# Kernel optimization log

Hardware: AMD Instinct MI355X
Metric: run time of the kernel (lower is better)

## Reference

```python
import jax, jax.numpy as jnp
import numpy as np

B = 1024      # Monte-Carlo samples (batch)
NX, NY = 8, 8 # lattice size
I = 3         # local Hilbert dim (hole, down, up)
H = 256       # hidden_dim
N_TARGET = 48 # target particle number
SZ = 0        # target magnetization sector


def setup_inputs() -> dict:
    key = jax.random.key(0)
    ks = jax.random.split(key, 8)
    f = jnp.float32
    samples = jax.random.randint(ks[0], (B, NX, NY), 0, 3)
    s_in = 1.0 / np.sqrt(2 * H)
    W1 = jax.random.normal(ks[1], (2 * I, 2 * H, H), f) * s_in
    W2 = jax.random.normal(ks[2], (2 * I, 2 * H, H), f) * s_in
    Wmerge = jax.random.normal(ks[3], (2 * H, H), f) * s_in
    b1 = jnp.full((H,), 0.01, f)
    b2 = jnp.full((H,), 0.01, f)
    s_l = 1.0 / np.sqrt(H)
    Wl1 = jax.random.normal(ks[4], (H, I), f) * s_l
    bl1 = jnp.zeros((I,), f)
    Wl2 = jax.random.normal(ks[5], (H, I), f) * s_l
    bl2 = jnp.zeros((I,), f)
    return {"samples": samples, "W1": W1, "b1": b1, "W2": W2, "b2": b2,
            "Wmerge": Wmerge, "Wl1": Wl1, "bl1": bl1, "Wl2": Wl2, "bl2": bl2}


def _gru_cell(sx, sy, hx, hy, W1, b1, W2, b2, Wmerge):
    # sx,sy: [B,I] one-hot neighbor inputs; hx,hy: [B,H] neighbor hiddens
    st = jnp.concatenate([hx, hy], axis=1)   # [B, 2H]
    inp = jnp.concatenate([sx, sy], axis=1)  # [B, 2I]
    # torch: einsum('ijk,lj->ikl', W, st) then einsum('li,ikl->lk', inp, .)
    pre1 = jnp.einsum('li,ijk,lj->lk', inp, W1, st)
    h_tilde = jnp.tanh(pre1 + b1)
    pre2 = jnp.einsum('li,ijk,lj->lk', inp, W2, st)
    u = jax.nn.sigmoid(pre2 + b2)
    return u * h_tilde + (1.0 - u) * (st @ Wmerge)


def _forward(samples, W1, b1, W2, b2, Wmerge, Wl1, bl1, Wl2, bl2):
    f = W1.dtype
    oh = jax.nn.one_hot(samples, I, dtype=f)  # [B,NX,NY,I]
    z_h = jnp.zeros((B, H), f)
    z_s = jnp.zeros((B, I), f)
    hid = {}
    bl_up = (N_TARGET + 2 * SZ) // 2
    bl_dn = (N_TARGET - 2 * SZ) // 2
    bl_hole = NX * NY - N_TARGET
    n_up = jnp.zeros((B,), f)
    n_dn = jnp.zeros((B,), f)
    log_a = jnp.zeros((B,), f)
    log_p = jnp.zeros((B,), f)
    k = 0  # number of already-sampled sites (static per step)
    for ny in range(NY):
        # snake (zig-zag) ordering over the 2D lattice
        xs = range(NX) if ny % 2 == 0 else range(NX - 1, -1, -1)
        dx = -1 if ny % 2 == 0 else 1
        for nx in xs:
            nxn = nx + dx
            sx = oh[:, nxn, ny] if 0 <= nxn < NX else z_s
            hx = hid.get((nxn, ny), z_h)
            sy = oh[:, nx, ny - 1] if ny > 0 else z_s
            hy = hid.get((nx, ny - 1), z_h)
            h = _gru_cell(sx, sy, hx, hy, W1, b1, W2, b2, Wmerge)
            hid[(nx, ny)] = h
            probs = jax.nn.softmax(h @ Wl1 + bl1, axis=1)          # [B,I]
            phase = jnp.pi * jax.nn.soft_sign(h @ Wl2 + bl2)       # [B,I]
            # enforce particle-number / magnetization sectors (heaviside masks)
            m_up = (bl_up - n_up > 0).astype(f)
            m_dn = (bl_dn - n_dn > 0).astype(f)
            m_hole = (bl_hole - (k - n_up - n_dn) > 0).astype(f)
            mask = jnp.stack([m_hole, m_dn, m_up], axis=1)         # [B,I]
            amp = probs * mask
            amp = amp / jnp.maximum(amp.sum(axis=1, keepdims=True), 1e-30)
            s = samples[:, nx, ny]
            sel = jax.nn.one_hot(s, I, dtype=f)
            log_a = log_a + jnp.log(jnp.clip((amp * sel).sum(axis=1), 1e-12))
            log_p = log_p + (phase * sel).sum(axis=1)
            n_up = n_up + (s == 2).astype(f)
            n_dn = n_dn + (s == 1).astype(f)
            k += 1
    return 0.5 * log_a, log_p


def reference(samples, W1, b1, W2, b2, Wmerge, Wl1, bl1, Wl2, bl2):
    return _forward(samples, W1, b1, W2, b2, Wmerge, Wl1, bl1, Wl2, bl2)
```

## Files before the change

kernel.cpp:

```cpp
#include <hip/hip_runtime.h>
#include <hip/hip_bf16.h>
#include <math.h>

#define Bsz 1024
#define Hd  256
#define MAXTILE 40
#define PERM_PER_CELL (MAXTILE*32)
#define WTSTRIDE (768*512)
#define GHALF (Bsz*768)
#define NPART 4

typedef short bf16x8 __attribute__((ext_vector_type(8)));
typedef float f32x4  __attribute__((ext_vector_type(4)));

__global__ __launch_bounds__(256)
void build_wc(const float* __restrict__ W1, const float* __restrict__ W2,
              const float* __restrict__ Wm,
              __hip_bfloat16* __restrict__ Wht, __hip_bfloat16* __restrict__ Wlt)
{
    size_t idx = (size_t)blockIdx.x * 256 + threadIdx.x;
    int k = (int)(idx & 511);
    size_t rem = idx >> 9;
    int col = (int)(rem % 768);
    int c = (int)(rem / 768);
    int a = c >> 2, b = c & 3;
    float v;
    if (col < 256) {
        v = ((a < 3) ? W1[(size_t)a * 512 * 256 + k * 256 + col] : 0.f)
          + ((b < 3) ? W1[(size_t)(3 + b) * 512 * 256 + k * 256 + col] : 0.f);
    } else if (col < 512) {
        int cc = col - 256;
        v = ((a < 3) ? W2[(size_t)a * 512 * 256 + k * 256 + cc] : 0.f)
          + ((b < 3) ? W2[(size_t)(3 + b) * 512 * 256 + k * 256 + cc] : 0.f);
    } else {
        v = Wm[(size_t)k * 256 + (col - 512)];
    }
    __hip_bfloat16 vh = __float2bfloat16(v);
    __hip_bfloat16 vl = __float2bfloat16(v - __bfloat162float(vh));
    Wht[idx] = vh;
    Wlt[idx] = vl;
}

__global__ __launch_bounds__(256)
void bucketize(const int* __restrict__ samples, int* __restrict__ perm,
               int* __restrict__ tiletab)
{
    const int cell = blockIdx.x;
    const int t = threadIdx.x;
    const int ny = cell >> 3, ixs = cell & 7;
    const int nx  = (ny & 1) ? (7 - ixs) : ixs;
    const int dx  = (ny & 1) ? 1 : -1;
    const int nxn = nx + dx;
    const bool hasX = (nxn >= 0) && (nxn < 8);
    const bool hasY = (ny > 0);
    const int sx_off = nxn * 8 + ny;
    const int sy_off = nx * 8 + ny - 1;

    __shared__ int hist[16], cursor[16];
    int* pcell = perm + (size_t)cell * PERM_PER_CELL;
    for (int i = t; i < PERM_PER_CELL; i += 256) pcell[i] = -1;
    if (t < 16) hist[t] = 0;
    __syncthreads();

    int myc[4];
#pragma unroll
    for (int q = 0; q < 4; q++) {
        int l = t * 4 + q;
        int a = hasX ? samples[l * 64 + sx_off] : 3;
        int b = hasY ? samples[l * 64 + sy_off] : 3;
        myc[q] = a * 4 + b;
        atomicAdd(&hist[myc[q]], 1);
    }
    __syncthreads();

    if (t == 0) {
        int tile = 0, row = 0;
        for (int c = 0; c < 16; c++) {
            cursor[c] = row;
            int nt = (hist[c] + 31) >> 5;
            for (int k = 0; k < nt; k++) tiletab[cell * MAXTILE + tile + k] = c;
            tile += nt;
            row  += nt * 32;
        }
        for (; tile < MAXTILE; tile++) tiletab[cell * MAXTILE + tile] = -1;
    }
    __syncthreads();

#pragma unroll
    for (int q = 0; q < 4; q++) {
        int l = t * 4 + q;
        int pos = atomicAdd(&cursor[myc[q]], 1);
        pcell[pos] = l;
    }
}

__global__ __launch_bounds__(256)
void gemm_mfma(const __hip_bfloat16* __restrict__ hxh, const __hip_bfloat16* __restrict__ hxl,
               const __hip_bfloat16* __restrict__ hyh, const __hip_bfloat16* __restrict__ hyl,
               const __hip_bfloat16* __restrict__ Wht, const __hip_bfloat16* __restrict__ Wlt,
               const int* __restrict__ perm, const int* __restrict__ tiletab,
               float* __restrict__ Gp, int cell, int kbeg, int kend)
{
    const int combo = tiletab[cell * MAXTILE + blockIdx.y];
    if (combo < 0) return;
    const int chunk = blockIdx.z;
    const int kbase = chunk << 7;
    const int lo = (kbeg > kbase) ? kbeg : kbase;
    const int hi = (kend < kbase + 128) ? kend : (kbase + 128);
    const int k0 = blockIdx.x * 64;
    const int* pr = perm + (size_t)cell * PERM_PER_CELL + blockIdx.y * 32;
    float* Gout = Gp + (size_t)chunk * GHALF;

    const int t  = threadIdx.x;
    const int w  = t >> 6;
    const int l  = t & 63;
    const int lr = l & 15;
    const int lg = l >> 4;

    __shared__ __align__(16) short Bh[64 * 128];
    __shared__ __align__(16) short Bl[64 * 128];

    f32x4 acc0 = {0.f, 0.f, 0.f, 0.f};
    f32x4 acc1 = {0.f, 0.f, 0.f, 0.f};

    if (lo < hi) {
        const __hip_bfloat16* baseH = Wht + (size_t)combo * WTSTRIDE + kbase;
        const __hip_bfloat16* baseL = Wlt + (size_t)combo * WTSTRIDE + kbase;
        for (int i = t; i < 1024; i += 256) {
            int c  = i >> 4;
            int kq = i & 15;
            int q  = c * 16 + (kq ^ (c & 7));
            ((uint4*)Bh)[q] = *(const uint4*)(baseH + (size_t)(k0 + c) * 512 + kq * 8);
            ((uint4*)Bl)[q] = *(const uint4*)(baseL + (size_t)(k0 + c) * 512 + kq * 8);
        }
        __syncthreads();

        const __hip_bfloat16* Hh = (chunk < 2) ? hxh : hyh;
        const __hip_bfloat16* Hl = (chunk < 2) ? hxl : hyl;
        const int hbase = kbase - ((chunk < 2) ? 0 : 256);
        const int r0 = pr[lr];
        const int r1 = pr[16 + lr];
        const int cB = w * 16 + lr;

#pragma unroll
        for (int ks = 0; ks < 4; ks++) {
            const int koff = hbase + ks * 32 + lg * 8;
            bf16x8 a0h = (r0 >= 0) ? *(const bf16x8*)(Hh + (size_t)r0 * Hd + koff) : (bf16x8)0;
            bf16x8 a0l = (r0 >= 0) ? *(const bf16x8*)(Hl + (size_t)r0 * Hd + koff) : (bf16x8)0;
            bf16x8 a1h = (r1 >= 0) ? *(const bf16x8*)(Hh + (size_t)r1 * Hd + koff) : (bf16x8)0;
            bf16x8 a1l = (r1 >= 0) ? *(const bf16x8*)(Hl + (size_t)r1 * Hd + koff) : (bf16x8)0;

            const int kq = ks * 4 + lg;
            const int q  = cB * 16 + (kq ^ (cB & 7));
            bf16x8 bh = ((const bf16x8*)Bh)[q];
            bf16x8 bl = ((const bf16x8*)Bl)[q];

            acc0 = __builtin_amdgcn_mfma_f32_16x16x32_bf16(a0h, bh, acc0, 0, 0, 0);
            acc0 = __builtin_amdgcn_mfma_f32_16x16x32_bf16(a0h, bl, acc0, 0, 0, 0);
            acc0 = __builtin_amdgcn_mfma_f32_16x16x32_bf16(a0l, bh, acc0, 0, 0, 0);
            acc1 = __builtin_amdgcn_mfma_f32_16x16x32_bf16(a1h, bh, acc1, 0, 0, 0);
            acc1 = __builtin_amdgcn_mfma_f32_16x16x32_bf16(a1h, bl, acc1, 0, 0, 0);
            acc1 = __builtin_amdgcn_mfma_f32_16x16x32_bf16(a1l, bh, acc1, 0, 0, 0);
        }
    }

    const int colA = k0 + w * 16 + lr;
#pragma unroll
    for (int reg = 0; reg < 4; reg++) {
        const int rl = 4 * lg + reg;
        int ra = pr[rl];
        if (ra >= 0) Gout[(size_t)ra * 768 + colA] = acc0[reg];
        int rb = pr[16 + rl];
        if (rb >= 0) Gout[(size_t)rb * 768 + colA] = acc1[reg];
    }
}

__global__ __launch_bounds__(256)
void combine_logprob(const float* __restrict__ Gp, const int* __restrict__ samples,
                     const float* __restrict__ b1, const float* __restrict__ b2,
                     const float* __restrict__ Wl1, const float* __restrict__ bl1,
                     const float* __restrict__ Wl2, const float* __restrict__ bl2,
                     __hip_bfloat16* __restrict__ houth, __hip_bfloat16* __restrict__ houtl,
                     float* __restrict__ acc, float* __restrict__ out,
                     int s_off, int kcell)
{
    const int l = blockIdx.x;
    const int k = threadIdx.x;
    const float* g0 = Gp + (size_t)l * 768;

    float pre1 = b1[k], pre2 = b2[k], mg = 0.f;
#pragma unroll
    for (int z = 0; z < NPART; z++) {
        const float* g = g0 + (size_t)z * GHALF;
        pre1 += g[k];
        pre2 += g[256 + k];
        mg   += g[512 + k];
    }
    float ht = tanhf(pre1);
    float u  = 1.0f / (1.0f + expf(-pre2));
    float h  = u * ht + (1.0f - u) * mg;
    __hip_bfloat16 hh = __float2bfloat16(h);
    __hip_bfloat16 hl = __float2bfloat16(h - __bfloat162float(hh));
    houth[(size_t)l * Hd + k] = hh;
    houtl[(size_t)l * Hd + k] = hl;

    float v[6];
    v[0] = h * Wl1[k * 3 + 0];
    v[1] = h * Wl1[k * 3 + 1];
    v[2] = h * Wl1[k * 3 + 2];
    v[3] = h * Wl2[k * 3 + 0];
    v[4] = h * Wl2[k * 3 + 1];
    v[5] = h * Wl2[k * 3 + 2];
#pragma unroll
    for (int m = 1; m < 64; m <<= 1)
#pragma unroll
        for (int i = 0; i < 6; i++) v[i] += __shfl_xor(v[i], m);

    __shared__ float red[4][6];
    if ((k & 63) == 0) {
#pragma unroll
        for (int i = 0; i < 6; i++) red[k >> 6][i] = v[i];
    }
    __syncthreads();

    if (k == 0) {
        float p1[3], p2[3];
#pragma unroll
        for (int i = 0; i < 3; i++) {
            p1[i] = red[0][i]     + red[1][i]     + red[2][i]     + red[3][i];
            p2[i] = red[0][3 + i] + red[1][3 + i] + red[2][3 + i] + red[3][3 + i];
        }
        float la, lp, nu, nd;
        if (kcell == 0) { la = 0.f; lp = 0.f; nu = 0.f; nd = 0.f; }
        else {
            la = acc[l];           lp = acc[Bsz + l];
            nu = acc[2 * Bsz + l]; nd = acc[3 * Bsz + l];
        }
        float z0 = p1[0] + bl1[0], z1 = p1[1] + bl1[1], z2 = p1[2] + bl1[2];
        float zm = fmaxf(z0, fmaxf(z1, z2));
        float e0 = expf(z0 - zm), e1 = expf(z1 - zm), e2 = expf(z2 - zm);
        float es = e0 + e1 + e2;
        float mh = (16.0f - ((float)kcell - nu - nd) > 0.0f) ? 1.0f : 0.0f;
        float md = (24.0f - nd > 0.0f) ? 1.0f : 0.0f;
        float mu = (24.0f - nu > 0.0f) ? 1.0f : 0.0f;
        float a0 = (e0 / es) * mh, a1 = (e1 / es) * md, a2 = (e2 / es) * mu;
        float asum = fmaxf(a0 + a1 + a2, 1e-30f);
        int sv = samples[l * 64 + s_off];
        float av = ((sv == 0) ? a0 : (sv == 1) ? a1 : a2) / asum;
        float q  = p2[sv] + bl2[sv];
        float ph = 3.14159265358979323846f * (q / (1.0f + fabsf(q)));
        la += logf(fmaxf(av, 1e-12f));
        lp += ph;
        nu += (sv == 2) ? 1.0f : 0.0f;
        nd += (sv == 1) ? 1.0f : 0.0f;
        acc[l] = la; acc[Bsz + l] = lp;
        acc[2 * Bsz + l] = nu; acc[3 * Bsz + l] = nd;
        if (kcell == 63) {
            out[l]       = 0.5f * la;
            out[Bsz + l] = lp;
        }
    }
}

extern "C" void kernel_launch(void* const* d_in, const int* in_sizes, int n_in,
                              void* d_out, int out_size, void* d_ws, size_t ws_size,
                              hipStream_t stream)
{
    const int*   samples = (const int*)  d_in[0];
    const float* W1  = (const float*)d_in[1];
    const float* b1  = (const float*)d_in[2];
    const float* W2  = (const float*)d_in[3];
    const float* b2  = (const float*)d_in[4];
    const float* Wm  = (const float*)d_in[5];
    const float* Wl1 = (const float*)d_in[6];
    const float* bl1 = (const float*)d_in[7];
    const float* Wl2 = (const float*)d_in[8];
    const float* bl2 = (const float*)d_in[9];

    float* ws = (float*)d_ws;
    float* Gp  = ws;
    float* acc = Gp + (size_t)NPART * GHALF;
    __hip_bfloat16* Hh  = (__hip_bfloat16*)(acc + 4 * Bsz);
    __hip_bfloat16* Hl  = Hh + (size_t)8 * Bsz * Hd;
    __hip_bfloat16* Wht = Hl + (size_t)8 * Bsz * Hd;
    __hip_bfloat16* Wlt = Wht + (size_t)16 * WTSTRIDE;
    int* perm    = (int*)(Wlt + (size_t)16 * WTSTRIDE);
    int* tiletab = perm + (size_t)64 * PERM_PER_CELL;
    float* out = (float*)d_out;

    build_wc<<<dim3(16 * 768 * 512 / 256), dim3(256), 0, stream>>>(W1, W2, Wm, Wht, Wlt);
    bucketize<<<dim3(64), dim3(256), 0, stream>>>(samples, perm, tiletab);

    int kcell = 0;
    for (int ny = 0; ny < 8; ny++) {
        const int x0  = (ny % 2 == 0) ? 0 : 7;
        const int dxs = (ny % 2 == 0) ? 1 : -1;
        const int dx  = (ny % 2 == 0) ? -1 : 1;
        for (int ix = 0; ix < 8; ix++) {
            const int nx  = x0 + ix * dxs;
            const int nxn = nx + dx;
            const bool hasX = (nxn >= 0 && nxn < 8);
            const bool hasY = (ny > 0);
            const __hip_bfloat16* hxh = hasX ? (Hh + (size_t)nxn * Bsz * Hd) : nullptr;
            const __hip_bfloat16* hxl = hasX ? (Hl + (size_t)nxn * Bsz * Hd) : nullptr;
            const __hip_bfloat16* hyh = hasY ? (Hh + (size_t)nx  * Bsz * Hd) : nullptr;
            const __hip_bfloat16* hyl = hasY ? (Hl + (size_t)nx  * Bsz * Hd) : nullptr;
            const int kbeg = hasX ? 0   : 256;
            const int kend = hasY ? 512 : 256;

            gemm_mfma<<<dim3(12, MAXTILE, NPART), dim3(256), 0, stream>>>(
                hxh, hxl, hyh, hyl, Wht, Wlt, perm, tiletab, Gp, kcell, kbeg, kend);

            combine_logprob<<<dim3(Bsz), dim3(256), 0, stream>>>(
                Gp, samples, b1, b2, Wl1, bl1, Wl2, bl2,
                Hh + (size_t)nx * Bsz * Hd, Hl + (size_t)nx * Bsz * Hd,
                acc, out, nx * 8 + ny, kcell);
            kcell++;
        }
    }
}
```

Measured before the change: 1.958 ms.

## Replace 32-row tiles with 128-row segments reusing LDS weights across rows

Each GEMM block now loads a 64x256 weight slice for one neighbour half into LDS and loops over up to 128 rows of a combo segment. The old scheme reloaded a 64x128 slice for every 32-row tile across four K-chunks. This cuts redundant weight loads from global memory, drops the K-split from four partials to two, and skips blocks and partial reads for a missing neighbour. The cost is fewer blocks (12x17x2), a per-block row loop with less parallelism, and double the LDS per block (64 KB), which may lower occupancy.

```diff
diff --git a/kernel.cpp b/kernel.cpp
--- a/kernel.cpp
+++ b/kernel.cpp
@@ -4,11 +4,9 @@
 
 #define Bsz 1024
 #define Hd  256
-#define MAXTILE 40
-#define PERM_PER_CELL (MAXTILE*32)
+#define MAXSEG 17
 #define WTSTRIDE (768*512)
 #define GHALF (Bsz*768)
-#define NPART 4
 
 typedef short bf16x8 __attribute__((ext_vector_type(8)));
 typedef float f32x4  __attribute__((ext_vector_type(4)));
@@ -43,7 +41,7 @@
 
 __global__ __launch_bounds__(256)
 void bucketize(const int* __restrict__ samples, int* __restrict__ perm,
-               int* __restrict__ tiletab)
+               int* __restrict__ segtab)
 {
     const int cell = blockIdx.x;
     const int t = threadIdx.x;
@@ -57,8 +55,7 @@
     const int sy_off = nx * 8 + ny - 1;
 
     __shared__ int hist[16], cursor[16];
-    int* pcell = perm + (size_t)cell * PERM_PER_CELL;
-    for (int i = t; i < PERM_PER_CELL; i += 256) pcell[i] = -1;
+    int* pcell = perm + (size_t)cell * Bsz;
     if (t < 16) hist[t] = 0;
     __syncthreads();
 
@@ -74,15 +71,16 @@
     __syncthreads();
 
     if (t == 0) {
-        int tile = 0, row = 0;
+        int row = 0, ns = 0;
         for (int c = 0; c < 16; c++) {
             cursor[c] = row;
-            int nt = (hist[c] + 31) >> 5;
-            for (int k = 0; k < nt; k++) tiletab[cell * MAXTILE + tile + k] = c;
-            tile += nt;
-            row  += nt * 32;
-        }
-        for (; tile < MAXTILE; tile++) tiletab[cell * MAXTILE + tile] = -1;
+            for (int s = 0; s < hist[c]; s += 128) {
+                int cnt = hist[c] - s; if (cnt > 128) cnt = 128;
+                segtab[cell * MAXSEG + ns++] = (c << 18) | ((row + s) << 8) | cnt;
+            }
+            row += hist[c];
+        }
+        for (; ns < MAXSEG; ns++) segtab[cell * MAXSEG + ns] = -1;
     }
     __syncthreads();
 
@@ -95,21 +93,24 @@
 }
 
 __global__ __launch_bounds__(256)
-void gemm_mfma(const __hip_bfloat16* __restrict__ hxh, const __hip_bfloat16* __restrict__ hxl,
-               const __hip_bfloat16* __restrict__ hyh, const __hip_bfloat16* __restrict__ hyl,
+void gemm_mfma(const __hip_bfloat16* __restrict__ Hxh, const __hip_bfloat16* __restrict__ Hxl,
+               const __hip_bfloat16* __restrict__ Hyh, const __hip_bfloat16* __restrict__ Hyl,
                const __hip_bfloat16* __restrict__ Wht, const __hip_bfloat16* __restrict__ Wlt,
-               const int* __restrict__ perm, const int* __restrict__ tiletab,
-               float* __restrict__ Gp, int cell, int kbeg, int kend)
-{
-    const int combo = tiletab[cell * MAXTILE + blockIdx.y];
-    if (combo < 0) return;
-    const int chunk = blockIdx.z;
-    const int kbase = chunk << 7;
-    const int lo = (kbeg > kbase) ? kbeg : kbase;
-    const int hi = (kend < kbase + 128) ? kend : (kbase + 128);
-    const int k0 = blockIdx.x * 64;
-    const int* pr = perm + (size_t)cell * PERM_PER_CELL + blockIdx.y * 32;
-    float* Gout = Gp + (size_t)chunk * GHALF;
+               const int* __restrict__ perm, const int* __restrict__ segtab,
+               float* __restrict__ Gp, int cell, int hasX, int hasY)
+{
+    const int kh = blockIdx.z;
+    if ((kh ? hasY : hasX) == 0) return;
+    const int seg = segtab[cell * MAXSEG + blockIdx.y];
+    if (seg < 0) return;
+    const int combo = seg >> 18;
+    const int rs    = (seg >> 8) & 1023;
+    const int cnt   = seg & 255;
+    const int k0    = blockIdx.x * 64;
+    const int* pr   = perm + (size_t)cell * Bsz;
+    float* Gout     = Gp + (size_t)kh * GHALF;
+    const __hip_bfloat16* Hh = kh ? Hyh : Hxh;
+    const __hip_bfloat16* Hl = kh ? Hyl : Hxl;
 
     const int t  = threadIdx.x;
     const int w  = t >> 6;
@@ -117,41 +118,43 @@
     const int lr = l & 15;
     const int lg = l >> 4;
 
-    __shared__ __align__(16) short Bh[64 * 128];
-    __shared__ __align__(16) short Bl[64 * 128];
-
-    f32x4 acc0 = {0.f, 0.f, 0.f, 0.f};
-    f32x4 acc1 = {0.f, 0.f, 0.f, 0.f};
-
-    if (lo < hi) {
-        const __hip_bfloat16* baseH = Wht + (size_t)combo * WTSTRIDE + kbase;
-        const __hip_bfloat16* baseL = Wlt + (size_t)combo * WTSTRIDE + kbase;
-        for (int i = t; i < 1024; i += 256) {
-            int c  = i >> 4;
-            int kq = i & 15;
-            int q  = c * 16 + (kq ^ (c & 7));
+    __shared__ __align__(16) short Bh[64 * 256];
+    __shared__ __align__(16) short Bl[64 * 256];
+
+    {
+        const __hip_bfloat16* baseH = Wht + (size_t)combo * WTSTRIDE + kh * 256;
+        const __hip_bfloat16* baseL = Wlt + (size_t)combo * WTSTRIDE + kh * 256;
+        for (int i = t; i < 2048; i += 256) {
+            int c  = i >> 5;
+            int kq = i & 31;
+            int q  = c * 32 + (kq ^ (c & 7));
             ((uint4*)Bh)[q] = *(const uint4*)(baseH + (size_t)(k0 + c) * 512 + kq * 8);
             ((uint4*)Bl)[q] = *(const uint4*)(baseL + (size_t)(k0 + c) * 512 + kq * 8);
         }
-        __syncthreads();
-
-        const __hip_bfloat16* Hh = (chunk < 2) ? hxh : hyh;
-        const __hip_bfloat16* Hl = (chunk < 2) ? hxl : hyl;
-        const int hbase = kbase - ((chunk < 2) ? 0 : 256);
-        const int r0 = pr[lr];
-        const int r1 = pr[16 + lr];
-        const int cB = w * 16 + lr;
-
-#pragma unroll
-        for (int ks = 0; ks < 4; ks++) {
-            const int koff = hbase + ks * 32 + lg * 8;
-            bf16x8 a0h = (r0 >= 0) ? *(const bf16x8*)(Hh + (size_t)r0 * Hd + koff) : (bf16x8)0;
-            bf16x8 a0l = (r0 >= 0) ? *(const bf16x8*)(Hl + (size_t)r0 * Hd + koff) : (bf16x8)0;
-            bf16x8 a1h = (r1 >= 0) ? *(const bf16x8*)(Hh + (size_t)r1 * Hd + koff) : (bf16x8)0;
-            bf16x8 a1l = (r1 >= 0) ? *(const bf16x8*)(Hl + (size_t)r1 * Hd + koff) : (bf16x8)0;
+    }
+    __syncthreads();
+
+    const int cB = w * 16 + lr;
+
+    for (int r0 = 0; r0 < cnt; r0 += 32) {
+        const int l0 = r0 + lr;
+        const int l1 = r0 + 16 + lr;
+        const int r0row = (l0 < cnt) ? pr[rs + l0] : -1;
+        const int r1row = (l1 < cnt) ? pr[rs + l1] : -1;
+
+        f32x4 acc0 = {0.f, 0.f, 0.f, 0.f};
+        f32x4 acc1 = {0.f, 0.f, 0.f, 0.f};
+
+#pragma unroll
+        for (int ks = 0; ks < 8; ks++) {
+            const int koff = ks * 32 + lg * 8;
+            bf16x8 a0h = (r0row >= 0) ? *(const bf16x8*)(Hh + (size_t)r0row * Hd + koff) : (bf16x8)0;
+            bf16x8 a0l = (r0row >= 0) ? *(const bf16x8*)(Hl + (size_t)r0row * Hd + koff) : (bf16x8)0;
+            bf16x8 a1h = (r1row >= 0) ? *(const bf16x8*)(Hh + (size_t)r1row * Hd + koff) : (bf16x8)0;
+            bf16x8 a1l = (r1row >= 0) ? *(const bf16x8*)(Hl + (size_t)r1row * Hd + koff) : (bf16x8)0;
 
             const int kq = ks * 4 + lg;
-            const int q  = cB * 16 + (kq ^ (cB & 7));
+            const int q  = cB * 32 + (kq ^ (cB & 7));
             bf16x8 bh = ((const bf16x8*)Bh)[q];
             bf16x8 bl = ((const bf16x8*)Bl)[q];
 
@@ -162,16 +165,21 @@
             acc1 = __builtin_amdgcn_mfma_f32_16x16x32_bf16(a1h, bl, acc1, 0, 0, 0);
             acc1 = __builtin_amdgcn_mfma_f32_16x16x32_bf16(a1l, bh, acc1, 0, 0, 0);
         }
-    }
-
-    const int colA = k0 + w * 16 + lr;
-#pragma unroll
-    for (int reg = 0; reg < 4; reg++) {
-        const int rl = 4 * lg + reg;
-        int ra = pr[rl];
-        if (ra >= 0) Gout[(size_t)ra * 768 + colA] = acc0[reg];
-        int rb = pr[16 + rl];
-        if (rb >= 0) Gout[(size_t)rb * 768 + colA] = acc1[reg];
+
+        const int colA = k0 + w * 16 + lr;
+#pragma unroll
+        for (int reg = 0; reg < 4; reg++) {
+            const int rlA = r0 + 4 * lg + reg;
+            if (rlA < cnt) {
+                int ra = pr[rs + rlA];
+                Gout[(size_t)ra * 768 + colA] = acc0[reg];
+            }
+            const int rlB = r0 + 16 + 4 * lg + reg;
+            if (rlB < cnt) {
+                int rb = pr[rs + rlB];
+                Gout[(size_t)rb * 768 + colA] = acc1[reg];
+            }
+        }
     }
 }
 
@@ -182,19 +190,19 @@
                      const float* __restrict__ Wl2, const float* __restrict__ bl2,
                      __hip_bfloat16* __restrict__ houth, __hip_bfloat16* __restrict__ houtl,
                      float* __restrict__ acc, float* __restrict__ out,
-                     int s_off, int kcell)
+                     int s_off, int kcell, int mask)
 {
     const int l = blockIdx.x;
     const int k = threadIdx.x;
-    const float* g0 = Gp + (size_t)l * 768;
 
     float pre1 = b1[k], pre2 = b2[k], mg = 0.f;
-#pragma unroll
-    for (int z = 0; z < NPART; z++) {
-        const float* g = g0 + (size_t)z * GHALF;
-        pre1 += g[k];
-        pre2 += g[256 + k];
-        mg   += g[512 + k];
+    if (mask & 1) {
+        const float* g = Gp + (size_t)l * 768;
+        pre1 += g[k]; pre2 += g[256 + k]; mg += g[512 + k];
+    }
+    if (mask & 2) {
+        const float* g = Gp + (size_t)GHALF + (size_t)l * 768;
+        pre1 += g[k]; pre2 += g[256 + k]; mg += g[512 + k];
     }
     float ht = tanhf(pre1);
     float u  = 1.0f / (1.0f + expf(-pre2));
@@ -279,17 +287,17 @@
 
     float* ws = (float*)d_ws;
     float* Gp  = ws;
-    float* acc = Gp + (size_t)NPART * GHALF;
+    float* acc = Gp + (size_t)2 * GHALF;
     __hip_bfloat16* Hh  = (__hip_bfloat16*)(acc + 4 * Bsz);
     __hip_bfloat16* Hl  = Hh + (size_t)8 * Bsz * Hd;
     __hip_bfloat16* Wht = Hl + (size_t)8 * Bsz * Hd;
     __hip_bfloat16* Wlt = Wht + (size_t)16 * WTSTRIDE;
-    int* perm    = (int*)(Wlt + (size_t)16 * WTSTRIDE);
-    int* tiletab = perm + (size_t)64 * PERM_PER_CELL;
+    int* perm   = (int*)(Wlt + (size_t)16 * WTSTRIDE);
+    int* segtab = perm + (size_t)64 * Bsz;
     float* out = (float*)d_out;
 
     build_wc<<<dim3(16 * 768 * 512 / 256), dim3(256), 0, stream>>>(W1, W2, Wm, Wht, Wlt);
-    bucketize<<<dim3(64), dim3(256), 0, stream>>>(samples, perm, tiletab);
+    bucketize<<<dim3(64), dim3(256), 0, stream>>>(samples, perm, segtab);
 
     int kcell = 0;
     for (int ny = 0; ny < 8; ny++) {
@@ -301,20 +309,22 @@
             const int nxn = nx + dx;
             const bool hasX = (nxn >= 0 && nxn < 8);
             const bool hasY = (ny > 0);
-            const __hip_bfloat16* hxh = hasX ? (Hh + (size_t)nxn * Bsz * Hd) : nullptr;
-            const __hip_bfloat16* hxl = hasX ? (Hl + (size_t)nxn * Bsz * Hd) : nullptr;
-            const __hip_bfloat16* hyh = hasY ? (Hh + (size_t)nx  * Bsz * Hd) : nullptr;
-            const __hip_bfloat16* hyl = hasY ? (Hl + (size_t)nx  * Bsz * Hd) : nullptr;
-            const int kbeg = hasX ? 0   : 256;
-            const int kend = hasY ? 512 : 256;
-
-            gemm_mfma<<<dim3(12, MAXTILE, NPART), dim3(256), 0, stream>>>(
-                hxh, hxl, hyh, hyl, Wht, Wlt, perm, tiletab, Gp, kcell, kbeg, kend);
+            const int mask = (hasX ? 1 : 0) | (hasY ? 2 : 0);
+
+            if (mask) {
+                const __hip_bfloat16* hxh = hasX ? (Hh + (size_t)nxn * Bsz * Hd) : Hh;
+                const __hip_bfloat16* hxl = hasX ? (Hl + (size_t)nxn * Bsz * Hd) : Hl;
+                const __hip_bfloat16* hyh = hasY ? (Hh + (size_t)nx  * Bsz * Hd) : Hh;
+                const __hip_bfloat16* hyl = hasY ? (Hl + (size_t)nx  * Bsz * Hd) : Hl;
+                gemm_mfma<<<dim3(12, MAXSEG, 2), dim3(256), 0, stream>>>(
+                    hxh, hxl, hyh, hyl, Wht, Wlt, perm, segtab, Gp,
+                    kcell, hasX ? 1 : 0, hasY ? 1 : 0);
+            }
 
             combine_logprob<<<dim3(Bsz), dim3(256), 0, stream>>>(
                 Gp, samples, b1, b2, Wl1, bl1, Wl2, bl2,
                 Hh + (size_t)nx * Bsz * Hd, Hl + (size_t)nx * Bsz * Hd,
-                acc, out, nx * 8 + ny, kcell);
+                acc, out, nx * 8 + ny, kcell, mask);
             kcell++;
         }
     }
```

Measured after the change: 2.697 ms. +37.7%, slower.

## Fuse per-cell GEMM and GRU/logprob epilogue into one kernel with 16-row tiles

Applied to the files above, without the earlier changes.

Replaces the split-K GEMM kernel plus separate combine kernel with a single fused kernel per lattice cell. Each 1024-thread block takes a 16-row bucket and computes all 768 output columns over the full K range, then does the GRU gating, hidden-state write and log-prob reduction in-block. This removes the Gp partial-sum round trip through global memory and one launch per cell. Hidden states are now double-buffered by row parity so the cell can read its own column's previous-row hidden state while writing the new one. In exchange, B weights are read directly from global memory without LDS staging, only up to 72 blocks run per launch, and the serial K loop per block is longer.

```diff
diff --git a/kernel.cpp b/kernel.cpp
--- a/kernel.cpp
+++ b/kernel.cpp
@@ -4,11 +4,8 @@
 
 #define Bsz 1024
 #define Hd  256
-#define MAXTILE 40
-#define PERM_PER_CELL (MAXTILE*32)
+#define MAXT 72
 #define WTSTRIDE (768*512)
-#define GHALF (Bsz*768)
-#define NPART 4
 
 typedef short bf16x8 __attribute__((ext_vector_type(8)));
 typedef float f32x4  __attribute__((ext_vector_type(4)));
@@ -42,8 +39,8 @@
 }
 
 __global__ __launch_bounds__(256)
-void bucketize(const int* __restrict__ samples, int* __restrict__ perm,
-               int* __restrict__ tiletab)
+void bucketize16(const int* __restrict__ samples, int* __restrict__ perm,
+                 int* __restrict__ tiletab)
 {
     const int cell = blockIdx.x;
     const int t = threadIdx.x;
@@ -57,8 +54,8 @@
     const int sy_off = nx * 8 + ny - 1;
 
     __shared__ int hist[16], cursor[16];
-    int* pcell = perm + (size_t)cell * PERM_PER_CELL;
-    for (int i = t; i < PERM_PER_CELL; i += 256) pcell[i] = -1;
+    int* pcell = perm + (size_t)cell * (MAXT * 16);
+    for (int i = t; i < MAXT * 16; i += 256) pcell[i] = -1;
     if (t < 16) hist[t] = 0;
     __syncthreads();
 
@@ -74,15 +71,14 @@
     __syncthreads();
 
     if (t == 0) {
-        int tile = 0, row = 0;
+        int row = 0, ns = 0;
         for (int c = 0; c < 16; c++) {
             cursor[c] = row;
-            int nt = (hist[c] + 31) >> 5;
-            for (int k = 0; k < nt; k++) tiletab[cell * MAXTILE + tile + k] = c;
-            tile += nt;
-            row  += nt * 32;
+            int nt = (hist[c] + 15) >> 4;
+            for (int k = 0; k < nt; k++) tiletab[cell * MAXT + ns++] = c;
+            row += nt * 16;
         }
-        for (; tile < MAXTILE; tile++) tiletab[cell * MAXTILE + tile] = -1;
+        for (; ns < MAXT; ns++) tiletab[cell * MAXT + ns] = -1;
     }
     __syncthreads();
 
@@ -94,22 +90,22 @@
     }
 }
 
-__global__ __launch_bounds__(256)
-void gemm_mfma(const __hip_bfloat16* __restrict__ hxh, const __hip_bfloat16* __restrict__ hxl,
-               const __hip_bfloat16* __restrict__ hyh, const __hip_bfloat16* __restrict__ hyl,
-               const __hip_bfloat16* __restrict__ Wht, const __hip_bfloat16* __restrict__ Wlt,
-               const int* __restrict__ perm, const int* __restrict__ tiletab,
-               float* __restrict__ Gp, int cell, int kbeg, int kend)
+__global__ __launch_bounds__(1024)
+void fused_cell(const __hip_bfloat16* __restrict__ Hxh, const __hip_bfloat16* __restrict__ Hxl,
+                const __hip_bfloat16* __restrict__ Hyh, const __hip_bfloat16* __restrict__ Hyl,
+                const __hip_bfloat16* __restrict__ Wht, const __hip_bfloat16* __restrict__ Wlt,
+                const float* __restrict__ b1, const float* __restrict__ b2,
+                const float* __restrict__ Wl1, const float* __restrict__ bl1,
+                const float* __restrict__ Wl2, const float* __restrict__ bl2,
+                const int* __restrict__ perm16, const int* __restrict__ tiletab16,
+                const int* __restrict__ samples,
+                __hip_bfloat16* __restrict__ Houth, __hip_bfloat16* __restrict__ Houtl,
+                float* __restrict__ acc, float* __restrict__ out,
+                int cell, int s_off, int kcell, int ksb, int kse)
 {
-    const int combo = tiletab[cell * MAXTILE + blockIdx.y];
+    const int combo = tiletab16[cell * MAXT + blockIdx.x];
     if (combo < 0) return;
-    const int chunk = blockIdx.z;
-    const int kbase = chunk << 7;
-    const int lo = (kbeg > kbase) ? kbeg : kbase;
-    const int hi = (kend < kbase + 128) ? kend : (kbase + 128);
-    const int k0 = blockIdx.x * 64;
-    const int* pr = perm + (size_t)cell * PERM_PER_CELL + blockIdx.y * 32;
-    float* Gout = Gp + (size_t)chunk * GHALF;
+    const int* pr = perm16 + ((size_t)cell * MAXT + blockIdx.x) * 16;
 
     const int t  = threadIdx.x;
     const int w  = t >> 6;
@@ -117,147 +113,135 @@
     const int lr = l & 15;
     const int lg = l >> 4;
 
-    __shared__ __align__(16) short Bh[64 * 128];
-    __shared__ __align__(16) short Bl[64 * 128];
-
-    f32x4 acc0 = {0.f, 0.f, 0.f, 0.f};
-    f32x4 acc1 = {0.f, 0.f, 0.f, 0.f};
-
-    if (lo < hi) {
-        const __hip_bfloat16* baseH = Wht + (size_t)combo * WTSTRIDE + kbase;
-        const __hip_bfloat16* baseL = Wlt + (size_t)combo * WTSTRIDE + kbase;
-        for (int i = t; i < 1024; i += 256) {
-            int c  = i >> 4;
-            int kq = i & 15;
-            int q  = c * 16 + (kq ^ (c & 7));
-            ((uint4*)Bh)[q] = *(const uint4*)(baseH + (size_t)(k0 + c) * 512 + kq * 8);
-            ((uint4*)Bl)[q] = *(const uint4*)(baseL + (size_t)(k0 + c) * 512 + kq * 8);
+    const int myrow = pr[lr];
+    const int col   = w * 16 + lr;
+
+    f32x4 ac0 = {0.f,0.f,0.f,0.f};
+    f32x4 ac1 = {0.f,0.f,0.f,0.f};
+    f32x4 ac2 = {0.f,0.f,0.f,0.f};
+
+    const __hip_bfloat16* B0h = Wht + (size_t)combo * WTSTRIDE + (size_t)col * 512;
+    const __hip_bfloat16* B0l = Wlt + (size_t)combo * WTSTRIDE + (size_t)col * 512;
+    const __hip_bfloat16* B1h = B0h + (size_t)256 * 512;
+    const __hip_bfloat16* B1l = B0l + (size_t)256 * 512;
+    const __hip_bfloat16* B2h = B0h + (size_t)512 * 512;
+    const __hip_bfloat16* B2l = B0l + (size_t)512 * 512;
+
+    for (int ks = ksb; ks < kse; ks++) {
+        const __hip_bfloat16* Ah_ = (ks < 8) ? Hxh : Hyh;
+        const __hip_bfloat16* Al_ = (ks < 8) ? Hxl : Hyl;
+        const int koff = ((ks & 7) * 32) + lg * 8;
+        bf16x8 ah = (myrow >= 0) ? *(const bf16x8*)(Ah_ + (size_t)myrow * Hd + koff) : (bf16x8)0;
+        bf16x8 al = (myrow >= 0) ? *(const bf16x8*)(Al_ + (size_t)myrow * Hd + koff) : (bf16x8)0;
+        const int kw = ks * 32 + lg * 8;
+        bf16x8 b0h = *(const bf16x8*)(B0h + kw);
+        bf16x8 b0l = *(const bf16x8*)(B0l + kw);
+        bf16x8 b1h = *(const bf16x8*)(B1h + kw);
+        bf16x8 b1l = *(const bf16x8*)(B1l + kw);
+        bf16x8 b2h = *(const bf16x8*)(B2h + kw);
+        bf16x8 b2l = *(const bf16x8*)(B2l + kw);
+
+        ac0 = __builtin_amdgcn_mfma_f32_16x16x32_bf16(ah, b0h, ac0, 0, 0, 0);
+        ac0 = __builtin_amdgcn_mfma_f32_16x16x32_bf16(ah, b0l, ac0, 0, 0, 0);
+        ac0 = __builtin_amdgcn_mfma_f32_16x16x32_bf16(al, b0h, ac0, 0, 0, 0);
+        ac1 = __builtin_amdgcn_mfma_f32_16x16x32_bf16(ah, b1h, ac1, 0, 0, 0);
+        ac1 = __builtin_amdgcn_mfma_f32_16x16x32_bf16(ah, b1l, ac1, 0, 0, 0);
+        ac1 = __builtin_amdgcn_mfma_f32_16x16x32_bf16(al, b1h, ac1, 0, 0, 0);
+        ac2 = __builtin_amdgcn_mfma_f32_16x16x32_bf16(ah, b2h, ac2, 0, 0, 0);
+        ac2 = __builtin_amdgcn_mfma_f32_16x16x32_bf16(ah, b2l, ac2, 0, 0, 0);
+        ac2 = __builtin_amdgcn_mfma_f32_16x16x32_bf16(al, b2h, ac2, 0, 0, 0);
+    }
+
+    const float bb1 = b1[col], bb2 = b2[col];
+    float hv[4];
+#pragma unroll
+    for (int reg = 0; reg < 4; reg++) {
+        int r = pr[4 * lg + reg];
+        float pre1 = ac0[reg] + bb1;
+        float pre2 = ac1[reg] + bb2;
+        float mg   = ac2[reg];
+        float th = tanhf(pre1);
+        float u  = 1.0f / (1.0f + expf(-pre2));
+        float h  = u * th + (1.0f - u) * mg;
+        hv[reg] = h;
+        if (r >= 0) {
+            __hip_bfloat16 hh = __float2bfloat16(h);
+            __hip_bfloat16 hl = __float2bfloat16(h - __bfloat162float(hh));
+            Houth[(size_t)r * Hd + col] = hh;
+            Houtl[(size_t)r * Hd + col] = hl;
         }
-        __syncthreads();
-
-        const __hip_bfloat16* Hh = (chunk < 2) ? hxh : hyh;
-        const __hip_bfloat16* Hl = (chunk < 2) ? hxl : hyl;
-        const int hbase = kbase - ((chunk < 2) ? 0 : 256);
-        const int r0 = pr[lr];
-        const int r1 = pr[16 + lr];
-        const int cB = w * 16 + lr;
-
-#pragma unroll
-        for (int ks = 0; ks < 4; ks++) {
-            const int koff = hbase + ks * 32 + lg * 8;
-            bf16x8 a0h = (r0 >= 0) ? *(const bf16x8*)(Hh + (size_t)r0 * Hd + koff) : (bf16x8)0;
-            bf16x8 a0l = (r0 >= 0) ? *(const bf16x8*)(Hl + (size_t)r0 * Hd + koff) : (bf16x8)0;
-            bf16x8 a1h = (r1 >= 0) ? *(const bf16x8*)(Hh + (size_t)r1 * Hd + koff) : (bf16x8)0;
-            bf16x8 a1l = (r1 >= 0) ? *(const bf16x8*)(Hl + (size_t)r1 * Hd + koff) : (bf16x8)0;
-
-            const int kq = ks * 4 + lg;
-            const int q  = cB * 16 + (kq ^ (cB & 7));
-            bf16x8 bh = ((const bf16x8*)Bh)[q];
-            bf16x8 bl = ((const bf16x8*)Bl)[q];
-
-            acc0 = __builtin_amdgcn_mfma_f32_16x16x32_bf16(a0h, bh, acc0, 0, 0, 0);
-            acc0 = __builtin_amdgcn_mfma_f32_16x16x32_bf16(a0h, bl, acc0, 0, 0, 0);
-            acc0 = __builtin_amdgcn_mfma_f32_16x16x32_bf16(a0l, bh, acc0, 0, 0, 0);
-            acc1 = __builtin_amdgcn_mfma_f32_16x16x32_bf16(a1h, bh, acc1, 0, 0, 0);
-            acc1 = __builtin_amdgcn_mfma_f32_16x16x32_bf16(a1h, bl, acc1, 0, 0, 0);
-            acc1 = __builtin_amdgcn_mfma_f32_16x16x32_bf16(a1l, bh, acc1, 0, 0, 0);
-        }
-    }
-
-    const int colA = k0 + w * 16 + lr;
+    }
+
+    float w1c0 = Wl1[col * 3 + 0], w1c1 = Wl1[col * 3 + 1], w1c2 = Wl1[col * 3 + 2];
+    float w2c0 = Wl2[col * 3 + 0], w2c1 = Wl2[col * 3 + 1], w2c2 = Wl2[col * 3 + 2];
+    float vr[4][6];
 #pragma unroll
     for (int reg = 0; reg < 4; reg++) {
-        const int rl = 4 * lg + reg;
-        int ra = pr[rl];
-        if (ra >= 0) Gout[(size_t)ra * 768 + colA] = acc0[reg];
-        int rb = pr[16 + rl];
-        if (rb >= 0) Gout[(size_t)rb * 768 + colA] = acc1[reg];
-    }
-}
-
-__global__ __launch_bounds__(256)
-void combine_logprob(const float* __restrict__ Gp, const int* __restrict__ samples,
-                     const float* __restrict__ b1, const float* __restrict__ b2,
-                     const float* __restrict__ Wl1, const float* __restrict__ bl1,
-                     const float* __restrict__ Wl2, const float* __restrict__ bl2,
-                     __hip_bfloat16* __restrict__ houth, __hip_bfloat16* __restrict__ houtl,
-                     float* __restrict__ acc, float* __restrict__ out,
-                     int s_off, int kcell)
-{
-    const int l = blockIdx.x;
-    const int k = threadIdx.x;
-    const float* g0 = Gp + (size_t)l * 768;
-
-    float pre1 = b1[k], pre2 = b2[k], mg = 0.f;
-#pragma unroll
-    for (int z = 0; z < NPART; z++) {
-        const float* g = g0 + (size_t)z * GHALF;
-        pre1 += g[k];
-        pre2 += g[256 + k];
-        mg   += g[512 + k];
-    }
-    float ht = tanhf(pre1);
-    float u  = 1.0f / (1.0f + expf(-pre2));
-    float h  = u * ht + (1.0f - u) * mg;
-    __hip_bfloat16 hh = __float2bfloat16(h);
-    __hip_bfloat16 hl = __float2bfloat16(h - __bfloat162float(hh));
-    houth[(size_t)l * Hd + k] = hh;
-    houtl[(size_t)l * Hd + k] = hl;
-
-    float v[6];
-    v[0] = h * Wl1[k * 3 + 0];
-    v[1] = h * Wl1[k * 3 + 1];
-    v[2] = h * Wl1[k * 3 + 2];
-    v[3] = h * Wl2[k * 3 + 0];
-    v[4] = h * Wl2[k * 3 + 1];
-    v[5] = h * Wl2[k * 3 + 2];
-#pragma unroll
-    for (int m = 1; m < 64; m <<= 1)
-#pragma unroll
-        for (int i = 0; i < 6; i++) v[i] += __shfl_xor(v[i], m);
-
-    __shared__ float red[4][6];
-    if ((k & 63) == 0) {
-#pragma unroll
-        for (int i = 0; i < 6; i++) red[k >> 6][i] = v[i];
-    }
-    __syncthreads();
-
-    if (k == 0) {
-        float p1[3], p2[3];
-#pragma unroll
-        for (int i = 0; i < 3; i++) {
-            p1[i] = red[0][i]     + red[1][i]     + red[2][i]     + red[3][i];
-            p2[i] = red[0][3 + i] + red[1][3 + i] + red[2][3 + i] + red[3][3 + i];
-        }
-        float la, lp, nu, nd;
-        if (kcell == 0) { la = 0.f; lp = 0.f; nu = 0.f; nd = 0.f; }
-        else {
-            la = acc[l];           lp = acc[Bsz + l];
-            nu = acc[2 * Bsz + l]; nd = acc[3 * Bsz + l];
-        }
-        float z0 = p1[0] + bl1[0], z1 = p1[1] + bl1[1], z2 = p1[2] + bl1[2];
-        float zm = fmaxf(z0, fmaxf(z1, z2));
-        float e0 = expf(z0 - zm), e1 = expf(z1 - zm), e2 = expf(z2 - zm);
-        float es = e0 + e1 + e2;
-        float mh = (16.0f - ((float)kcell - nu - nd) > 0.0f) ? 1.0f : 0.0f;
-        float md = (24.0f - nd > 0.0f) ? 1.0f : 0.0f;
-        float mu = (24.0f - nu > 0.0f) ? 1.0f : 0.0f;
-        float a0 = (e0 / es) * mh, a1 = (e1 / es) * md, a2 = (e2 / es) * mu;
-        float asum = fmaxf(a0 + a1 + a2, 1e-30f);
-        int sv = samples[l * 64 + s_off];
-        float av = ((sv == 0) ? a0 : (sv == 1) ? a1 : a2) / asum;
-        float q  = p2[sv] + bl2[sv];
-        float ph = 3.14159265358979323846f * (q / (1.0f + fabsf(q)));
-        la += logf(fmaxf(av, 1e-12f));
-        lp += ph;
-        nu += (sv == 2) ? 1.0f : 0.0f;
-        nd += (sv == 1) ? 1.0f : 0.0f;
-        acc[l] = la; acc[Bsz + l] = lp;
-        acc[2 * Bsz + l] = nu; acc[3 * Bsz + l] = nd;
-        if (kcell == 63) {
-            out[l]       = 0.5f * la;
-            out[Bsz + l] = lp;
+        vr[reg][0] = hv[reg] * w1c0; vr[reg][1] = hv[reg] * w1c1; vr[reg][2] = hv[reg] * w1c2;
+        vr[reg][3] = hv[reg] * w2c0; vr[reg][4] = hv[reg] * w2c1; vr[reg][5] = hv[reg] * w2c2;
+    }
+#pragma unroll
+    for (int m = 1; m < 16; m <<= 1)
+#pragma unroll
+        for (int reg = 0; reg < 4; reg++)
+#pragma unroll
+            for (int i = 0; i < 6; i++)
+                vr[reg][i] += __shfl_xor(vr[reg][i], m, 16);
+
+    __shared__ float red[16][16][6];
+    __shared__ float redS[16][6];
+    if (lr == 0) {
+#pragma unroll
+        for (int reg = 0; reg < 4; reg++)
+#pragma unroll
+            for (int i = 0; i < 6; i++)
+                red[w][4 * lg + reg][i] = vr[reg][i];
+    }
+    __syncthreads();
+
+    if (t < 96) {
+        int row = t / 6, i = t - row * 6;
+        float s = 0.f;
+#pragma unroll
+        for (int ww = 0; ww < 16; ww++) s += red[ww][row][i];
+        redS[row][i] = s;
+    }
+    __syncthreads();
+
+    if (t < 16) {
+        int r = pr[t];
+        if (r >= 0) {
+            float p1[3] = {redS[t][0], redS[t][1], redS[t][2]};
+            float p2[3] = {redS[t][3], redS[t][4], redS[t][5]};
+            float la, lp, nu, nd;
+            if (kcell == 0) { la = 0.f; lp = 0.f; nu = 0.f; nd = 0.f; }
+            else {
+                la = acc[r];           lp = acc[Bsz + r];
+                nu = acc[2 * Bsz + r]; nd = acc[3 * Bsz + r];
+            }
+            float z0 = p1[0] + bl1[0], z1 = p1[1] + bl1[1], z2 = p1[2] + bl1[2];
+            float zm = fmaxf(z0, fmaxf(z1, z2));
+            float e0 = expf(z0 - zm), e1 = expf(z1 - zm), e2 = expf(z2 - zm);
+            float es = e0 + e1 + e2;
+            float mh = (16.0f - ((float)kcell - nu - nd) > 0.0f) ? 1.0f : 0.0f;
+            float md = (24.0f - nd > 0.0f) ? 1.0f : 0.0f;
+            float mu = (24.0f - nu > 0.0f) ? 1.0f : 0.0f;
+            float a0 = (e0 / es) * mh, a1 = (e1 / es) * md, a2 = (e2 / es) * mu;
+            float asum = fmaxf(a0 + a1 + a2, 1e-30f);
+            int sv = samples[r * 64 + s_off];
+            float av = ((sv == 0) ? a0 : (sv == 1) ? a1 : a2) / asum;
+            float q  = p2[sv] + bl2[sv];
+            float ph = 3.14159265358979323846f * (q / (1.0f + fabsf(q)));
+            la += logf(fmaxf(av, 1e-12f));
+            lp += ph;
+            nu += (sv == 2) ? 1.0f : 0.0f;
+            nd += (sv == 1) ? 1.0f : 0.0f;
+            acc[r] = la; acc[Bsz + r] = lp;
+            acc[2 * Bsz + r] = nu; acc[3 * Bsz + r] = nd;
+            if (kcell == 63) {
+                out[r]       = 0.5f * la;
+                out[Bsz + r] = lp;
+            }
         }
     }
 }
@@ -278,18 +262,17 @@
     const float* bl2 = (const float*)d_in[9];
 
     float* ws = (float*)d_ws;
-    float* Gp  = ws;
-    float* acc = Gp + (size_t)NPART * GHALF;
+    float* acc = ws;
     __hip_bfloat16* Hh  = (__hip_bfloat16*)(acc + 4 * Bsz);
-    __hip_bfloat16* Hl  = Hh + (size_t)8 * Bsz * Hd;
-    __hip_bfloat16* Wht = Hl + (size_t)8 * Bsz * Hd;
+    __hip_bfloat16* Hl  = Hh + (size_t)16 * Bsz * Hd;
+    __hip_bfloat16* Wht = Hl + (size_t)16 * Bsz * Hd;
     __hip_bfloat16* Wlt = Wht + (size_t)16 * WTSTRIDE;
-    int* perm    = (int*)(Wlt + (size_t)16 * WTSTRIDE);
-    int* tiletab = perm + (size_t)64 * PERM_PER_CELL;
+    int* perm16   = (int*)(Wlt + (size_t)16 * WTSTRIDE);
+    int* tiletab16 = perm16 + (size_t)64 * MAXT * 16;
     float* out = (float*)d_out;
 
     build_wc<<<dim3(16 * 768 * 512 / 256), dim3(256), 0, stream>>>(W1, W2, Wm, Wht, Wlt);
-    bucketize<<<dim3(64), dim3(256), 0, stream>>>(samples, perm, tiletab);
+    bucketize16<<<dim3(64), dim3(256), 0, stream>>>(samples, perm16, tiletab16);
 
     int kcell = 0;
     for (int ny = 0; ny < 8; ny++) {
@@ -301,20 +284,19 @@
             const int nxn = nx + dx;
             const bool hasX = (nxn >= 0 && nxn < 8);
             const bool hasY = (ny > 0);
-            const __hip_bfloat16* hxh = hasX ? (Hh + (size_t)nxn * Bsz * Hd) : nullptr;
-            const __hip_bfloat16* hxl = hasX ? (Hl + (size_t)nxn * Bsz * Hd) : nullptr;
-            const __hip_bfloat16* hyh = hasY ? (Hh + (size_t)nx  * Bsz * Hd) : nullptr;
-            const __hip_bfloat16* hyl = hasY ? (Hl + (size_t)nx  * Bsz * Hd) : nullptr;
-            const int kbeg = hasX ? 0   : 256;
-            const int kend = hasY ? 512 : 256;
-
-            gemm_mfma<<<dim3(12, MAXTILE, NPART), dim3(256), 0, stream>>>(
-                hxh, hxl, hyh, hyl, Wht, Wlt, perm, tiletab, Gp, kcell, kbeg, kend);
-
-            combine_logprob<<<dim3(Bsz), dim3(256), 0, stream>>>(
-                Gp, samples, b1, b2, Wl1, bl1, Wl2, bl2,
-                Hh + (size_t)nx * Bsz * Hd, Hl + (size_t)nx * Bsz * Hd,
-                acc, out, nx * 8 + ny, kcell);
+            const int p   = ny & 1;
+            const size_t slotW  = ((size_t)nx * 2 + p) * Bsz * Hd;
+            const size_t slotX  = ((size_t)(hasX ? nxn : 0) * 2 + p) * Bsz * Hd;
+            const size_t slotY  = ((size_t)nx * 2 + (1 - p)) * Bsz * Hd;
+            const int ksb = hasX ? 0 : 8;
+            const int kse = hasY ? 16 : 8;
+
+            fused_cell<<<dim3(MAXT), dim3(1024), 0, stream>>>(
+                Hh + slotX, Hl + slotX, Hh + slotY, Hl + slotY,
+                Wht, Wlt, b1, b2, Wl1, bl1, Wl2, bl2,
+                perm16, tiletab16, samples,
+                Hh + slotW, Hl + slotW, acc, out,
+                kcell, nx * 8 + ny, kcell, ksb, kse);
             kcell++;
         }
     }
```

Result: slower. 3.676 ms (+87.7%).
